# Kernel optimization log

Measured on AMD Instinct MI355X. Metric: run time of the kernel, lower is better.

## Reference

```python
import jax, jax.numpy as jnp
import numpy as np

N = 50000   # nodes
E = 800000  # edges (before self-loops)
IN, HID, OUT = 128, 128, 64


def gcn_norm(edge_index, num_nodes):
    # add self loops with weight 1, then symmetric deg^-1/2 normalization
    loop = jnp.arange(num_nodes, dtype=edge_index.dtype)
    row = jnp.concatenate([edge_index[0], loop])
    col = jnp.concatenate([edge_index[1], loop])
    ew = jnp.ones(row.shape[0], dtype=jnp.float32)
    deg = jax.ops.segment_sum(ew, col, num_segments=num_nodes)
    dis = jnp.where(deg > 0, jax.lax.rsqrt(deg), 0.0)
    norm = dis[row] * ew * dis[col]
    return row, col, norm


def gcn_conv(x, row, col, norm, W, b):
    h = x @ W                                   # [N, F_out] dense GEMM
    msg = h[row] * norm[:, None]                # gather + scale over edges
    out = jax.ops.segment_sum(msg, col, num_segments=x.shape[0])  # scatter-add
    return out + b


def setup_inputs() -> dict:
    key = jax.random.key(0)
    k0, k1, k2, k3, k4, k5 = jax.random.split(key, 6)
    x = jax.random.normal(k0, (N, IN), dtype=jnp.float32)
    edge_index = jax.random.randint(k1, (2, E), 0, N, dtype=jnp.int32)
    # glorot-style init for linear weights, zeros for bias (PyG default)
    W1 = jax.random.normal(k2, (IN, HID), dtype=jnp.float32) * np.float32(np.sqrt(1.0 / IN))
    b1 = jnp.zeros((HID,), dtype=jnp.float32)
    W2 = jax.random.normal(k3, (HID, OUT), dtype=jnp.float32) * np.float32(np.sqrt(1.0 / HID))
    b2 = jnp.zeros((OUT,), dtype=jnp.float32)
    return {"x": x, "edge_index": edge_index, "W1": W1, "b1": b1, "W2": W2, "b2": b2}


def reference(x, edge_index, W1, b1, W2, b2):
    row, col, norm = gcn_norm(edge_index, x.shape[0])
    h = jax.nn.relu(gcn_conv(x, row, col, norm, W1, b1))
    # dropout is a no-op in eval mode (training=False)
    out = gcn_conv(h, row, col, norm, W2, b2)
    return out
```

## Files before the change

kernel.cpp:

```cpp
#include <hip/hip_runtime.h>
#include <hip/hip_fp16.h>


#define Nn 50000
#define Ne 800000
#define NE2 (Ne / 2)
#define SCAN_B ((Nn + 1023) / 1024)
#define GT ((Nn + 63) / 64)
#define EPB 512

using f16x8 = _Float16 __attribute__((ext_vector_type(8)));
using f32x4 = float __attribute__((ext_vector_type(4)));

__global__ __launch_bounds__(256) void k_prep(const float* __restrict__ W1,
                                              const float* __restrict__ W2,
                                              _Float16* __restrict__ W1h,
                                              _Float16* __restrict__ W2h,
                                              int* __restrict__ degi) {
  const int b = blockIdx.x, t = threadIdx.x;
  if (b < 49) {
    int i = b * 256 + t;
    if (i < Nn / 4) ((int4*)degi)[i] = make_int4(0, 0, 0, 0);
  } else if (b == 49) {
    for (int i = 0; i < 8; ++i) {
      int id = i * 256 + t;
      int c = id & 127, k8 = id >> 7;
      f16x8 hv;
      #pragma unroll
      for (int j = 0; j < 8; ++j) hv[j] = (_Float16)W1[(k8 * 8 + j) * 128 + c];
      *(f16x8*)&W1h[c * 128 + ((k8 ^ (c & 7)) << 3)] = hv;
    }
  } else {
    for (int i = 0; i < 4; ++i) {
      int id = i * 256 + t;
      int c = id & 63, k8 = id >> 6;
      f16x8 hv;
      #pragma unroll
      for (int j = 0; j < 8; ++j) hv[j] = (_Float16)W2[(k8 * 8 + j) * 64 + c];
      *(f16x8*)&W2h[c * 128 + ((k8 ^ (c & 7)) << 3)] = hv;
    }
  }
}

__global__ __launch_bounds__(256, 4) void k_gemm128_count(
    const float* __restrict__ X, const _Float16* __restrict__ W1h,
    __half* __restrict__ H, const int2* __restrict__ col2,
    int* __restrict__ degi, ushort2* __restrict__ rank2) {
  __shared__ _Float16 Wts[128 * 128];

  const int tid = threadIdx.x;
  const int base = blockIdx.x * 64;

  {
    const f16x8* src = (const f16x8*)W1h;
    f16x8* dst = (f16x8*)Wts;
    #pragma unroll
    for (int i = 0; i < 8; ++i) dst[i * 256 + tid] = src[i * 256 + tid];
  }

  {
    int i0 = blockIdx.x * EPB + tid;
    int i1 = i0 + 256;
    if (i0 < NE2) {
      int2 c = col2[i0];
      ushort2 rk;
      rk.x = (unsigned short)atomicAdd(&degi[c.x], 1);
      rk.y = (unsigned short)atomicAdd(&degi[c.y], 1);
      rank2[i0] = rk;
    }
    if (i1 < NE2) {
      int2 c = col2[i1];
      ushort2 rk;
      rk.x = (unsigned short)atomicAdd(&degi[c.x], 1);
      rk.y = (unsigned short)atomicAdd(&degi[c.y], 1);
      rank2[i1] = rk;
    }
  }

  const int w = tid >> 6, lane = tid & 63;
  const int quad = lane >> 4, mrow = lane & 15;
  int anode = base + w * 16 + mrow;
  if (anode >= Nn) anode = Nn - 1;
  const float4* xg = (const float4*)(X + (size_t)anode * 128);
  f16x8 av[4];
  #pragma unroll
  for (int ko = 0; ko < 4; ++ko) {
    float4 x0 = xg[ko * 8 + quad * 2];
    float4 x1 = xg[ko * 8 + quad * 2 + 1];
    av[ko][0] = (_Float16)x0.x; av[ko][1] = (_Float16)x0.y;
    av[ko][2] = (_Float16)x0.z; av[ko][3] = (_Float16)x0.w;
    av[ko][4] = (_Float16)x1.x; av[ko][5] = (_Float16)x1.y;
    av[ko][6] = (_Float16)x1.z; av[ko][7] = (_Float16)x1.w;
  }
  __syncthreads();

  f32x4 acc[8];
  #pragma unroll
  for (int ct = 0; ct < 8; ++ct) acc[ct] = (f32x4){0.f, 0.f, 0.f, 0.f};

  #pragma unroll
  for (int ko = 0; ko < 4; ++ko) {
    #pragma unroll
    for (int ct = 0; ct < 8; ++ct) {
      int c = ct * 16 + mrow;
      f16x8 bv = *(const f16x8*)&Wts[c * 128 + (((ko * 4 + quad) ^ (c & 7)) << 3)];
      acc[ct] = __builtin_amdgcn_mfma_f32_16x16x32_f16(av[ko], bv, acc[ct], 0, 0, 0);
    }
  }

  #pragma unroll
  for (int ct = 0; ct < 8; ++ct) {
    #pragma unroll
    for (int r = 0; r < 4; ++r) {
      int node = base + w * 16 + quad * 4 + r;
      if (node < Nn)
        H[(size_t)node * 128 + ct * 16 + mrow] = __float2half(acc[ct][r]);
    }
  }
}

__global__ __launch_bounds__(1024) void k_scan1(const int* __restrict__ degi,
                                                int* __restrict__ rowptr,
                                                float* __restrict__ dis,
                                                int* __restrict__ bsum) {
  __shared__ int wsum[16];
  int tid = threadIdx.x;
  int lane = tid & 63, wid = tid >> 6;
  int i = blockIdx.x * 1024 + tid;
  int v = (i < Nn) ? degi[i] : 0;
  if (i < Nn) dis[i] = rsqrtf((float)(v + 1));
  int incl = v;
  #pragma unroll
  for (int off = 1; off < 64; off <<= 1) {
    int t = __shfl_up(incl, off);
    if (lane >= off) incl += t;
  }
  if (lane == 63) wsum[wid] = incl;
  __syncthreads();
  if (wid == 0) {
    int wv = (lane < 16) ? wsum[lane] : 0;
    #pragma unroll
    for (int off = 1; off < 16; off <<= 1) {
      int t = __shfl_up(wv, off);
      if (lane >= off) wv += t;
    }
    if (lane < 16) wsum[lane] = wv;
  }
  __syncthreads();
  int woff = (wid > 0) ? wsum[wid - 1] : 0;
  if (i < Nn) rowptr[i] = woff + incl - v;
  if (tid == 0) bsum[blockIdx.x] = wsum[15];
}

__global__ __launch_bounds__(1024) void k_scan3(int* __restrict__ rowptr,
                                                const int* __restrict__ bsum) {
  __shared__ int off_s;
  int tid = threadIdx.x;
  if (tid < 64) {
    int v = (tid < SCAN_B) ? bsum[tid] : 0;
    int incl = v;
    #pragma unroll
    for (int off = 1; off < 64; off <<= 1) {
      int t = __shfl_up(incl, off);
      if (tid >= off) incl += t;
    }
    if (tid == (int)blockIdx.x) off_s = incl - v;
    if (blockIdx.x == 0 && tid == SCAN_B - 1) rowptr[Nn] = incl;
  }
  __syncthreads();
  int i = blockIdx.x * 1024 + tid;
  if (i < Nn) rowptr[i] += off_s;
}

__global__ __launch_bounds__(256) void k_fill(const int2* __restrict__ row2,
                                              const int2* __restrict__ col2,
                                              const int* __restrict__ rowptr,
                                              const ushort2* __restrict__ rank2,
                                              unsigned short* __restrict__ csr) {
  int t = blockIdx.x * 256 + threadIdx.x;
  if (t >= NE2) return;
  int2 r = row2[t];
  int2 c = col2[t];
  ushort2 k = rank2[t];
  csr[rowptr[c.x] + (int)k.x] = (unsigned short)r.x;
  csr[rowptr[c.y] + (int)k.y] = (unsigned short)r.y;
}

__device__ __forceinline__ float2 h2f(unsigned int u) {
  return __half22float2(*(const __half2*)&u);
}

__global__ __launch_bounds__(256) void k_agg128_gemm64(
    const __half* __restrict__ H, const unsigned short* __restrict__ csr,
    const int* __restrict__ rowptr, const float* __restrict__ dis,
    const float* __restrict__ bias, const _Float16* __restrict__ W2h,
    __half* __restrict__ H2, int n) {
  __shared__ _Float16 Wts[64 * 128];
  __shared__ _Float16 Hs[16 * 136];

  const int tid = threadIdx.x;
  const int wid = tid >> 6, lane = tid & 63;
  const int sub = lane >> 4, fl = lane & 15;
  const int nb = wid * 4 + sub;
  const int v = blockIdx.x * 16 + nb;

  {
    const f16x8* src = (const f16x8*)W2h;
    f16x8* dst = (f16x8*)Wts;
    #pragma unroll
    for (int i = 0; i < 4; ++i) dst[i * 256 + tid] = src[i * 256 + tid];
  }

  int s = rowptr[v], e = rowptr[v + 1];
  float d = dis[v];
  float sw = d * d;
  const uint4* Hq = (const uint4*)H;
  uint4 hv = Hq[(size_t)v * 16 + fl];
  float2 p0 = h2f(hv.x), p1 = h2f(hv.y), p2 = h2f(hv.z), p3 = h2f(hv.w);
  float a0 = p0.x * sw, a1 = p0.y * sw, a2 = p1.x * sw, a3 = p1.y * sw;
  float a4 = p2.x * sw, a5 = p2.y * sw, a6 = p3.x * sw, a7 = p3.y * sw;
  constexpr int D = 6;
  if (s < e) {
    int srcs[D];
    #pragma unroll
    for (int j = 0; j < D; ++j) {
      int idx = s + j;
      srcs[j] = csr[(idx < e) ? idx : (e - 1)];
    }
    for (int base = s; base < e; base += D) {
      uint4 q[D];
      float wd[D];
      #pragma unroll
      for (int j = 0; j < D; ++j) q[j] = Hq[(size_t)srcs[j] * 16 + fl];
      #pragma unroll
      for (int j = 0; j < D; ++j) wd[j] = dis[srcs[j]];
      int ns[D];
      #pragma unroll
      for (int j = 0; j < D; ++j) {
        int idx = base + D + j;
        ns[j] = csr[(idx < e) ? idx : (e - 1)];
      }
      #pragma unroll
      for (int j = 0; j < D; ++j) {
        float w = ((base + j) < e) ? wd[j] * d : 0.f;
        float2 t;
        t = h2f(q[j].x); a0 = fmaf(w, t.x, a0); a1 = fmaf(w, t.y, a1);
        t = h2f(q[j].y); a2 = fmaf(w, t.x, a2); a3 = fmaf(w, t.y, a3);
        t = h2f(q[j].z); a4 = fmaf(w, t.x, a4); a5 = fmaf(w, t.y, a5);
        t = h2f(q[j].w); a6 = fmaf(w, t.x, a6); a7 = fmaf(w, t.y, a7);
      }
      #pragma unroll
      for (int j = 0; j < D; ++j) srcs[j] = ns[j];
    }
  }
  {
    const float4* Bq = (const float4*)bias;
    float4 b0 = Bq[fl * 2], b1v = Bq[fl * 2 + 1];
    f16x8 hrow;
    hrow[0] = (_Float16)fmaxf(a0 + b0.x, 0.f);
    hrow[1] = (_Float16)fmaxf(a1 + b0.y, 0.f);
    hrow[2] = (_Float16)fmaxf(a2 + b0.z, 0.f);
    hrow[3] = (_Float16)fmaxf(a3 + b0.w, 0.f);
    hrow[4] = (_Float16)fmaxf(a4 + b1v.x, 0.f);
    hrow[5] = (_Float16)fmaxf(a5 + b1v.y, 0.f);
    hrow[6] = (_Float16)fmaxf(a6 + b1v.z, 0.f);
    hrow[7] = (_Float16)fmaxf(a7 + b1v.w, 0.f);
    *(f16x8*)&Hs[nb * 136 + fl * 8] = hrow;
  }
  __syncthreads();

  const int quad = lane >> 4, mrow = lane & 15;
  f32x4 acc = (f32x4){0.f, 0.f, 0.f, 0.f};
  const int c = wid * 16 + mrow;
  #pragma unroll
  for (int ko = 0; ko < 4; ++ko) {
    f16x8 avx = *(const f16x8*)&Hs[mrow * 136 + ko * 32 + quad * 8];
    f16x8 bv = *(const f16x8*)&Wts[c * 128 + (((ko * 4 + quad) ^ (c & 7)) << 3)];
    acc = __builtin_amdgcn_mfma_f32_16x16x32_f16(avx, bv, acc, 0, 0, 0);
  }
  #pragma unroll
  for (int r = 0; r < 4; ++r) {
    int node = blockIdx.x * 16 + quad * 4 + r;
    if (node < n)
      H2[(size_t)node * 64 + wid * 16 + mrow] = __float2half(acc[r]);
  }
}

__global__ __launch_bounds__(256) void k_agg64(const __half* __restrict__ H,
                                               const unsigned short* __restrict__ csr,
                                               const int* __restrict__ rowptr,
                                               const float* __restrict__ dis,
                                               const float* __restrict__ bias,
                                               float* __restrict__ Out, int n) {
  const int wid = threadIdx.x >> 6, lane = threadIdx.x & 63;
  const int sub = lane >> 4, fl = lane & 15;
  int v = blockIdx.x * 16 + wid * 4 + sub;
  if (v >= n) return;
  int s = rowptr[v], e = rowptr[v + 1];
  float d = dis[v];
  float sw = d * d;
  const uint2* Hq = (const uint2*)H;
  uint2 hv = Hq[(size_t)v * 16 + fl];
  float2 p0 = h2f(hv.x), p1 = h2f(hv.y);
  float a0 = p0.x * sw, a1 = p0.y * sw, a2 = p1.x * sw, a3 = p1.y * sw;
  constexpr int D = 8;
  if (s < e) {
    int srcs[D];
    #pragma unroll
    for (int j = 0; j < D; ++j) {
      int idx = s + j;
      srcs[j] = csr[(idx < e) ? idx : (e - 1)];
    }
    for (int base = s; base < e; base += D) {
      uint2 q[D];
      float wd[D];
      #pragma unroll
      for (int j = 0; j < D; ++j) q[j] = Hq[(size_t)srcs[j] * 16 + fl];
      #pragma unroll
      for (int j = 0; j < D; ++j) wd[j] = dis[srcs[j]];
      int ns[D];
      #pragma unroll
      for (int j = 0; j < D; ++j) {
        int idx = base + D + j;
        ns[j] = csr[(idx < e) ? idx : (e - 1)];
      }
      #pragma unroll
      for (int j = 0; j < D; ++j) {
        float w = ((base + j) < e) ? wd[j] * d : 0.f;
        float2 t;
        t = h2f(q[j].x); a0 = fmaf(w, t.x, a0); a1 = fmaf(w, t.y, a1);
        t = h2f(q[j].y); a2 = fmaf(w, t.x, a2); a3 = fmaf(w, t.y, a3);
      }
      #pragma unroll
      for (int j = 0; j < D; ++j) srcs[j] = ns[j];
    }
  }
  const float4* Bq = (const float4*)bias;
  float4 b = Bq[fl];
  float4 o = make_float4(a0 + b.x, a1 + b.y, a2 + b.z, a3 + b.w);
  ((float4*)(Out + (size_t)v * 64))[fl] = o;
}

extern "C" void kernel_launch(void* const* d_in, const int* in_sizes, int n_in,
                              void* d_out, int out_size, void* d_ws, size_t ws_size,
                              hipStream_t stream) {
  const float* x  = (const float*)d_in[0];
  const int*   ei = (const int*)d_in[1];
  const int*   row = ei;
  const int*   col = ei + Ne;
  const float* W1 = (const float*)d_in[2];
  const float* b1 = (const float*)d_in[3];
  const float* W2 = (const float*)d_in[4];
  const float* b2 = (const float*)d_in[5];
  float* out = (float*)d_out;

  char* ws = (char*)d_ws;
  size_t off = 0;
  auto alloc = [&](size_t bytes) -> void* {
    void* p = ws + off;
    off += (bytes + 255) & ~(size_t)255;
    return p;
  };
  int*    degi   = (int*)   alloc(Nn * sizeof(int));
  int*    rowptr = (int*)   alloc((Nn + 1) * sizeof(int));
  float*  dis    = (float*) alloc(Nn * sizeof(float));
  int*    bsum   = (int*)   alloc(64 * sizeof(int));
  unsigned short* rank = (unsigned short*)alloc((size_t)Ne * sizeof(unsigned short));
  unsigned short* csr  = (unsigned short*)alloc((size_t)Ne * sizeof(unsigned short));
  __half* H1     = (__half*)alloc((size_t)Nn * 128 * sizeof(__half));
  __half* H2     = (__half*)alloc((size_t)Nn * 64 * sizeof(__half));
  _Float16* W1h  = (_Float16*)alloc(128 * 128 * sizeof(_Float16));
  _Float16* W2h  = (_Float16*)alloc(64 * 128 * sizeof(_Float16));

  const int NGB = (Nn + 15) / 16;
  const int E1B = (NE2 + 255) / 256;

  k_prep<<<51, 256, 0, stream>>>(W1, W2, W1h, W2h, degi);
  k_gemm128_count<<<GT, 256, 0, stream>>>(x, W1h, H1, (const int2*)col,
                                          degi, (ushort2*)rank);
  k_scan1<<<SCAN_B, 1024, 0, stream>>>(degi, rowptr, dis, bsum);
  k_scan3<<<SCAN_B, 1024, 0, stream>>>(rowptr, bsum);
  k_fill<<<E1B, 256, 0, stream>>>((const int2*)row, (const int2*)col, rowptr,
                                  (const ushort2*)rank, csr);
  k_agg128_gemm64<<<NGB, 256, 0, stream>>>(H1, csr, rowptr, dis, b1, W2h, H2, Nn);
  k_agg64<<<NGB, 256, 0, stream>>>(H2, csr, rowptr, dis, b2, out, Nn);
}
```

Measured before the change: 186.5 us.

## Merge scan and CSR fill into one cooperative kernel; stage GEMM stores through LDS

The two scan kernels and the CSR fill kernel become one cooperative kernel that uses grid-wide syncs, removing two launches and their gaps. The first GEMM now uses 32-row tiles, with warps split across row and column halves, and writes its output through LDS so the H1 stores are coalesced 16-byte writes. The second-layer GEMM output in the aggregation kernel is staged through LDS the same way. The trade-offs are that the fill runs on only about 49 blocks in a strided loop, grid.sync has its own cost, and every GEMM block still reloads the full weight matrix, so there are twice as many weight loads.

```diff
diff --git a/kernel.cpp b/kernel.cpp
--- a/kernel.cpp
+++ b/kernel.cpp
@@ -1,13 +1,15 @@
 #include <hip/hip_runtime.h>
 #include <hip/hip_fp16.h>
+#include <hip/hip_cooperative_groups.h>
 
 
 #define Nn 50000
 #define Ne 800000
 #define NE2 (Ne / 2)
 #define SCAN_B ((Nn + 1023) / 1024)
-#define GT ((Nn + 63) / 64)
-#define EPB 512
+#define GT32 ((Nn + 31) / 32)
+
+namespace cg = cooperative_groups;
 
 using f16x8 = _Float16 __attribute__((ext_vector_type(8)));
 using f32x4 = float __attribute__((ext_vector_type(4)));
@@ -42,14 +44,15 @@
   }
 }
 
-__global__ __launch_bounds__(256, 4) void k_gemm128_count(
+__global__ __launch_bounds__(256, 5) void k_gemm32_count(
     const float* __restrict__ X, const _Float16* __restrict__ W1h,
     __half* __restrict__ H, const int2* __restrict__ col2,
     int* __restrict__ degi, ushort2* __restrict__ rank2) {
   __shared__ _Float16 Wts[128 * 128];
+  _Float16* Hsx = Wts;
 
   const int tid = threadIdx.x;
-  const int base = blockIdx.x * 64;
+  const int base = blockIdx.x * 32;
 
   {
     const f16x8* src = (const f16x8*)W1h;
@@ -59,8 +62,7 @@
   }
 
   {
-    int i0 = blockIdx.x * EPB + tid;
-    int i1 = i0 + 256;
+    int i0 = blockIdx.x * 256 + tid;
     if (i0 < NE2) {
       int2 c = col2[i0];
       ushort2 rk;
@@ -68,18 +70,12 @@
       rk.y = (unsigned short)atomicAdd(&degi[c.y], 1);
       rank2[i0] = rk;
     }
-    if (i1 < NE2) {
-      int2 c = col2[i1];
-      ushort2 rk;
-      rk.x = (unsigned short)atomicAdd(&degi[c.x], 1);
-      rk.y = (unsigned short)atomicAdd(&degi[c.y], 1);
-      rank2[i1] = rk;
-    }
   }
 
   const int w = tid >> 6, lane = tid & 63;
   const int quad = lane >> 4, mrow = lane & 15;
-  int anode = base + w * 16 + mrow;
+  const int rbase = (w & 1) * 16, cbase = (w >> 1) * 64;
+  int anode = base + rbase + mrow;
   if (anode >= Nn) anode = Nn - 1;
   const float4* xg = (const float4*)(X + (size_t)anode * 128);
   f16x8 av[4];
@@ -94,39 +90,53 @@
   }
   __syncthreads();
 
-  f32x4 acc[8];
-  #pragma unroll
-  for (int ct = 0; ct < 8; ++ct) acc[ct] = (f32x4){0.f, 0.f, 0.f, 0.f};
+  f32x4 acc[4];
+  #pragma unroll
+  for (int ct = 0; ct < 4; ++ct) acc[ct] = (f32x4){0.f, 0.f, 0.f, 0.f};
 
   #pragma unroll
   for (int ko = 0; ko < 4; ++ko) {
     #pragma unroll
-    for (int ct = 0; ct < 8; ++ct) {
-      int c = ct * 16 + mrow;
+    for (int ct = 0; ct < 4; ++ct) {
+      int c = cbase + ct * 16 + mrow;
       f16x8 bv = *(const f16x8*)&Wts[c * 128 + (((ko * 4 + quad) ^ (c & 7)) << 3)];
       acc[ct] = __builtin_amdgcn_mfma_f32_16x16x32_f16(av[ko], bv, acc[ct], 0, 0, 0);
     }
   }
 
-  #pragma unroll
-  for (int ct = 0; ct < 8; ++ct) {
-    #pragma unroll
-    for (int r = 0; r < 4; ++r) {
-      int node = base + w * 16 + quad * 4 + r;
-      if (node < Nn)
-        H[(size_t)node * 128 + ct * 16 + mrow] = __float2half(acc[ct][r]);
-    }
-  }
-}
-
-__global__ __launch_bounds__(1024) void k_scan1(const int* __restrict__ degi,
-                                                int* __restrict__ rowptr,
-                                                float* __restrict__ dis,
-                                                int* __restrict__ bsum) {
+  __syncthreads();
+  #pragma unroll
+  for (int ct = 0; ct < 4; ++ct) {
+    #pragma unroll
+    for (int r = 0; r < 4; ++r)
+      Hsx[(rbase + quad * 4 + r) * 136 + cbase + ct * 16 + mrow] =
+          (_Float16)acc[ct][r];
+  }
+  __syncthreads();
+
+  #pragma unroll
+  for (int i = 0; i < 2; ++i) {
+    int id = i * 256 + tid;
+    int r = id >> 4, ch = id & 15;
+    int node = base + r;
+    if (node < Nn)
+      *(f16x8*)((_Float16*)H + (size_t)node * 128 + ch * 8) =
+          *(const f16x8*)&Hsx[r * 136 + ch * 8];
+  }
+}
+
+__global__ __launch_bounds__(1024) void k_scanfill(
+    const int* __restrict__ degi, int* __restrict__ rowptr,
+    float* __restrict__ dis, int* __restrict__ bsum,
+    const int2* __restrict__ row2, const int2* __restrict__ col2,
+    const ushort2* __restrict__ rank2, unsigned short* __restrict__ csr) {
+  cg::grid_group grid = cg::this_grid();
   __shared__ int wsum[16];
-  int tid = threadIdx.x;
-  int lane = tid & 63, wid = tid >> 6;
-  int i = blockIdx.x * 1024 + tid;
+  __shared__ int off_s;
+  const int tid = threadIdx.x;
+  const int lane = tid & 63, wid = tid >> 6;
+  const int i = blockIdx.x * 1024 + tid;
+
   int v = (i < Nn) ? degi[i] : 0;
   if (i < Nn) dis[i] = rsqrtf((float)(v + 1));
   int incl = v;
@@ -148,42 +158,32 @@
   }
   __syncthreads();
   int woff = (wid > 0) ? wsum[wid - 1] : 0;
-  if (i < Nn) rowptr[i] = woff + incl - v;
+  int local = woff + incl - v;
   if (tid == 0) bsum[blockIdx.x] = wsum[15];
-}
-
-__global__ __launch_bounds__(1024) void k_scan3(int* __restrict__ rowptr,
-                                                const int* __restrict__ bsum) {
-  __shared__ int off_s;
-  int tid = threadIdx.x;
+  grid.sync();
+
   if (tid < 64) {
-    int v = (tid < SCAN_B) ? bsum[tid] : 0;
-    int incl = v;
+    int bv = (tid < SCAN_B) ? bsum[tid] : 0;
+    int binc = bv;
     #pragma unroll
     for (int off = 1; off < 64; off <<= 1) {
-      int t = __shfl_up(incl, off);
-      if (tid >= off) incl += t;
-    }
-    if (tid == (int)blockIdx.x) off_s = incl - v;
-    if (blockIdx.x == 0 && tid == SCAN_B - 1) rowptr[Nn] = incl;
-  }
-  __syncthreads();
-  int i = blockIdx.x * 1024 + tid;
-  if (i < Nn) rowptr[i] += off_s;
-}
-
-__global__ __launch_bounds__(256) void k_fill(const int2* __restrict__ row2,
-                                              const int2* __restrict__ col2,
-                                              const int* __restrict__ rowptr,
-                                              const ushort2* __restrict__ rank2,
-                                              unsigned short* __restrict__ csr) {
-  int t = blockIdx.x * 256 + threadIdx.x;
-  if (t >= NE2) return;
-  int2 r = row2[t];
-  int2 c = col2[t];
-  ushort2 k = rank2[t];
-  csr[rowptr[c.x] + (int)k.x] = (unsigned short)r.x;
-  csr[rowptr[c.y] + (int)k.y] = (unsigned short)r.y;
+      int t = __shfl_up(binc, off);
+      if (tid >= off) binc += t;
+    }
+    if (tid == (int)blockIdx.x) off_s = binc - bv;
+    if (blockIdx.x == 0 && tid == SCAN_B - 1) rowptr[Nn] = binc;
+  }
+  __syncthreads();
+  if (i < Nn) rowptr[i] = local + off_s;
+  grid.sync();
+
+  for (int t = blockIdx.x * 1024 + tid; t < NE2; t += SCAN_B * 1024) {
+    int2 r = row2[t];
+    int2 c = col2[t];
+    ushort2 k = rank2[t];
+    csr[rowptr[c.x] + (int)k.x] = (unsigned short)r.x;
+    csr[rowptr[c.y] + (int)k.y] = (unsigned short)r.y;
+  }
 }
 
 __device__ __forceinline__ float2 h2f(unsigned int u) {
@@ -278,11 +278,17 @@
     f16x8 bv = *(const f16x8*)&Wts[c * 128 + (((ko * 4 + quad) ^ (c & 7)) << 3)];
     acc = __builtin_amdgcn_mfma_f32_16x16x32_f16(avx, bv, acc, 0, 0, 0);
   }
-  #pragma unroll
-  for (int r = 0; r < 4; ++r) {
-    int node = blockIdx.x * 16 + quad * 4 + r;
-    if (node < n)
-      H2[(size_t)node * 64 + wid * 16 + mrow] = __float2half(acc[r]);
+
+  __syncthreads();
+  #pragma unroll
+  for (int r = 0; r < 4; ++r)
+    Hs[(quad * 4 + r) * 136 + wid * 16 + mrow] = (_Float16)acc[r];
+  __syncthreads();
+
+  if (tid < 128) {
+    int r = tid >> 3, ch = tid & 7;
+    *(f16x8*)((_Float16*)H2 + ((size_t)blockIdx.x * 16 + r) * 64 + ch * 8) =
+        *(const f16x8*)&Hs[r * 136 + ch * 8];
   }
 }
 
@@ -373,15 +379,19 @@
   _Float16* W2h  = (_Float16*)alloc(64 * 128 * sizeof(_Float16));
 
   const int NGB = (Nn + 15) / 16;
-  const int E1B = (NE2 + 255) / 256;
 
   k_prep<<<51, 256, 0, stream>>>(W1, W2, W1h, W2h, degi);
-  k_gemm128_count<<<GT, 256, 0, stream>>>(x, W1h, H1, (const int2*)col,
-                                          degi, (ushort2*)rank);
-  k_scan1<<<SCAN_B, 1024, 0, stream>>>(degi, rowptr, dis, bsum);
-  k_scan3<<<SCAN_B, 1024, 0, stream>>>(rowptr, bsum);
-  k_fill<<<E1B, 256, 0, stream>>>((const int2*)row, (const int2*)col, rowptr,
-                                  (const ushort2*)rank, csr);
+  k_gemm32_count<<<GT32, 256, 0, stream>>>(x, W1h, H1, (const int2*)col,
+                                           degi, (ushort2*)rank);
+  {
+    const int2* row2 = (const int2*)row;
+    const int2* col2 = (const int2*)col;
+    ushort2* rank2 = (ushort2*)rank;
+    void* args[] = {(void*)&degi, (void*)&rowptr, (void*)&dis, (void*)&bsum,
+                    (void*)&row2, (void*)&col2, (void*)&rank2, (void*)&csr};
+    hipLaunchCooperativeKernel((void*)k_scanfill, dim3(SCAN_B), dim3(1024),
+                               args, 0, stream);
+  }
   k_agg128_gemm64<<<NGB, 256, 0, stream>>>(H1, csr, rowptr, dis, b1, W2h, H2, Nn);
   k_agg64<<<NGB, 256, 0, stream>>>(H2, csr, rowptr, dis, b2, out, Nn);
 }
```

After: 245.8 us. 31.8% more time.
